# Kernel optimization log

Measured on AMD Instinct MI355X. Metric: run time of the kernel, lower is better.

Reference implementation:

```python
import jax, jax.numpy as jnp
import numpy as np

N_WINDOW = 128  # |i-j| < N_WINDOW kept
D_K = 64

def setup_inputs() -> dict:
    key = jax.random.key(0)
    kq, kk, kv = jax.random.split(key, 3)
    B, H, S, D = 2, 8, 2048, D_K
    Q = jax.random.normal(kq, (B, H, S, D), dtype=jnp.float32)
    K = jax.random.normal(kk, (B, H, S, D), dtype=jnp.float32)
    V = jax.random.normal(kv, (B, H, S, D), dtype=jnp.float32)
    return {"Q": Q, "K": K, "V": V}

def reference(Q, K, V):
    S = Q.shape[-2]
    # scores: [B, H, S, S]
    scores = jnp.einsum('bhqd,bhkd->bhqk', Q, K) / jnp.sqrt(jnp.float32(D_K))
    idx = jnp.arange(S)
    band = jnp.abs(idx[:, None] - idx[None, :]) < N_WINDOW  # [S, S] band mask
    scores = jnp.where(band[None, None, :, :], scores, -jnp.inf)
    attn = jax.nn.softmax(scores, axis=-1)
    context = jnp.einsum('bhqk,bhkd->bhqd', attn, V)
    return (context, attn)
```

## Files before the change

### kernel.cpp

```cpp
#include <hip/hip_runtime.h>
#include <hip/hip_bf16.h>
#include <math.h>

#define S_LEN 2048
#define DK 64
#define TQ 32
#define KLW 320
#define NCH 5
#define PSTR 324
#define PSTR4 81

typedef __attribute__((ext_vector_type(8))) short bf16x8;
typedef __attribute__((ext_vector_type(4))) float f32x4;

__device__ __forceinline__ bf16x8 pack8(f32x4 a, f32x4 b) {
    union { __hip_bfloat162 h[4]; bf16x8 v; } u;
    u.h[0] = __float22bfloat162_rn(make_float2(a[0], a[1]));
    u.h[1] = __float22bfloat162_rn(make_float2(a[2], a[3]));
    u.h[2] = __float22bfloat162_rn(make_float2(b[0], b[1]));
    u.h[3] = __float22bfloat162_rn(make_float2(b[2], b[3]));
    return u.v;
}

__global__ __launch_bounds__(256, 3) void band_attn_v6(
    const float* __restrict__ Q,
    const float* __restrict__ K,
    const float* __restrict__ V,
    float* __restrict__ ctx_out,
    float* __restrict__ attn_out)
{
    __shared__ __align__(16) float Ps[TQ * PSTR];

    const int tid  = threadIdx.x;
    const int bh   = blockIdx.x >> 6;
    const int q0   = (blockIdx.x & 63) * TQ;
    const int base = q0 - 128;

    const int lane = tid & 63;
    const int wv   = tid >> 6;
    const int col  = lane & 15;
    const int quad = lane >> 4;

    const float* Qh = Q + ((size_t)bh * S_LEN + q0) * DK;
    const float* Kh = K + (size_t)bh * S_LEN * DK;
    const float* Vh = V + (size_t)bh * S_LEN * DK;

    bf16x8 qf[2][2];
    #pragma unroll
    for (int qt = 0; qt < 2; ++qt)
        #pragma unroll
        for (int h = 0; h < 2; ++h) {
            const float* qp = Qh + (size_t)(16 * qt + col) * DK + 32 * h + 8 * quad;
            f32x4 a = *(const f32x4*)qp;
            f32x4 b = *(const f32x4*)(qp + 4);
            a *= 0.125f; b *= 0.125f;
            qf[qt][h] = pack8(a, b);
        }

    #pragma unroll
    for (int c = 0; c < NCH; ++c) {
        const int kl  = c * 64 + 16 * wv + col;
        const int kg  = base + kl;
        const int kgc = min(max(kg, 0), S_LEN - 1);
        bf16x8 kf[2];
        #pragma unroll
        for (int h = 0; h < 2; ++h) {
            const float* kp = Kh + (size_t)kgc * DK + 32 * h + 8 * quad;
            kf[h] = pack8(*(const f32x4*)kp, *(const f32x4*)(kp + 4));
        }
        #pragma unroll
        for (int qt = 0; qt < 2; ++qt) {
            f32x4 acc = {0.f, 0.f, 0.f, 0.f};
            acc = __builtin_amdgcn_mfma_f32_16x16x32_bf16(qf[qt][0], kf[0], acc, 0, 0, 0);
            acc = __builtin_amdgcn_mfma_f32_16x16x32_bf16(qf[qt][1], kf[1], acc, 0, 0, 0);
            #pragma unroll
            for (int r = 0; r < 4; ++r) {
                const int qloc = 16 * qt + quad * 4 + r;
                const bool ok = ((unsigned)kg < S_LEN) && (kl > qloc) && (kl <= qloc + 255);
                Ps[qloc * PSTR + kl] = ok ? acc[r] : -INFINITY;
            }
        }
    }

    const int kloff4 = (q0 >> 2) - 32;
    const int L = max(0, kloff4);
    const int R = min(512, kloff4 + (KLW >> 2));
    f32x4* A4w = (f32x4*)(attn_out + ((size_t)bh * S_LEN + q0 + 8 * wv) * S_LEN);
    {
        const f32x4 z = {0.f, 0.f, 0.f, 0.f};
        #pragma unroll
        for (int rr = 0; rr < 8; ++rr) {
            f32x4* row4 = A4w + (size_t)rr * 512;
            for (int s = lane; s < L; s += 64)       row4[s] = z;
            for (int s = R + lane; s < 512; s += 64) row4[s] = z;
        }
    }
    __syncthreads();

    #pragma unroll
    for (int rr = 0; rr < 8; ++rr) {
        float* row = Ps + (wv * 8 + rr) * PSTR;
        float v[5];
        #pragma unroll
        for (int j = 0; j < 5; ++j) v[j] = row[lane + 64 * j];
        float m = fmaxf(fmaxf(fmaxf(v[0], v[1]), fmaxf(v[2], v[3])), v[4]);
        #pragma unroll
        for (int off = 32; off > 0; off >>= 1) m = fmaxf(m, __shfl_xor(m, off, 64));
        float e[5], sum = 0.f;
        #pragma unroll
        for (int j = 0; j < 5; ++j) { e[j] = __expf(v[j] - m); sum += e[j]; }
        #pragma unroll
        for (int off = 32; off > 0; off >>= 1) sum += __shfl_xor(sum, off, 64);
        const float inv = 1.0f / sum;
        #pragma unroll
        for (int j = 0; j < 5; ++j) row[lane + 64 * j] = e[j] * inv;
    }
    __syncthreads();

    f32x4 o0 = {0.f, 0.f, 0.f, 0.f}, o1 = {0.f, 0.f, 0.f, 0.f};
    const float* vcol = Vh + 16 * wv + col;
    #pragma unroll
    for (int c = 0; c < NCH; ++c) {
        #pragma unroll
        for (int h = 0; h < 2; ++h) {
            const int k0 = base + c * 64 + 32 * h + 8 * quad;
            f32x4 va, vb;
            #pragma unroll
            for (int j = 0; j < 4; ++j) {
                int kgc = min(max(k0 + j, 0), S_LEN - 1);
                va[j] = vcol[(size_t)kgc * DK];
            }
            #pragma unroll
            for (int j = 0; j < 4; ++j) {
                int kgc = min(max(k0 + 4 + j, 0), S_LEN - 1);
                vb[j] = vcol[(size_t)kgc * DK];
            }
            bf16x8 vf = pack8(va, vb);
            #pragma unroll
            for (int qt = 0; qt < 2; ++qt) {
                const float* pp = Ps + (size_t)(16 * qt + col) * PSTR + c * 64 + 32 * h + 8 * quad;
                bf16x8 pf = pack8(*(const f32x4*)pp, *(const f32x4*)(pp + 4));
                if (qt == 0) o0 = __builtin_amdgcn_mfma_f32_16x16x32_bf16(pf, vf, o0, 0, 0, 0);
                else         o1 = __builtin_amdgcn_mfma_f32_16x16x32_bf16(pf, vf, o1, 0, 0, 0);
            }
        }
    }

    {
        float* Cg = ctx_out + ((size_t)bh * S_LEN + q0) * DK;
        #pragma unroll
        for (int r = 0; r < 4; ++r) {
            Cg[(size_t)(quad * 4 + r) * DK + 16 * wv + col]      = o0[r];
            Cg[(size_t)(16 + quad * 4 + r) * DK + 16 * wv + col] = o1[r];
        }
    }

    {
        const f32x4* Ps4 = (const f32x4*)Ps;
        #pragma unroll
        for (int rr = 0; rr < 8; ++rr) {
            f32x4* row4 = A4w + (size_t)rr * 512;
            const f32x4* pr = Ps4 + (8 * wv + rr) * PSTR4 - kloff4;
            for (int s = L + lane; s < R; s += 64) row4[s] = pr[s];
        }
    }
}

extern "C" void kernel_launch(void* const* d_in, const int* in_sizes, int n_in,
                              void* d_out, int out_size, void* d_ws, size_t ws_size,
                              hipStream_t stream) {
    const float* Q = (const float*)d_in[0];
    const float* K = (const float*)d_in[1];
    const float* V = (const float*)d_in[2];
    float* out = (float*)d_out;

    const int BH = in_sizes[0] / (S_LEN * DK);
    const size_t ctx_elems = (size_t)BH * S_LEN * DK;
    float* ctx  = out;
    float* attn = out + ctx_elems;

    dim3 grid(BH * (S_LEN / TQ));
    band_attn_v6<<<grid, 256, 0, stream>>>(Q, K, V, ctx, attn);
}
```

Before: 302.8 us.

## Stream band probabilities directly from softmax and stagger zero-fill by block parity

The band probabilities are now written to global memory straight from registers during softmax, using nontemporal scalar stores, instead of a final pass that copied them from shared memory as 16-byte vectors. The zero-fill of the out-of-band attention region also uses nontemporal stores. Odd blocks do this zero-fill before softmax and even blocks after the PV matmul, so write traffic is spread across kernel phases. The cost being targeted is the large attention-matrix write bandwidth and its poor overlap with compute. In exchange, band writes become scalar rather than vector, which may reduce store efficiency.

Measured after the change: 298.3 us. Within noise of the previous version (-1.5%).

```diff
diff --git a/kernel.cpp b/kernel.cpp
--- a/kernel.cpp
+++ b/kernel.cpp
@@ -22,7 +22,7 @@
     return u.v;
 }
 
-__global__ __launch_bounds__(256, 3) void band_attn_v6(
+__global__ __launch_bounds__(256, 3) void band_attn_v7(
     const float* __restrict__ Q,
     const float* __restrict__ K,
     const float* __restrict__ V,
@@ -35,6 +35,7 @@
     const int bh   = blockIdx.x >> 6;
     const int q0   = (blockIdx.x & 63) * TQ;
     const int base = q0 - 128;
+    const int cls  = blockIdx.x & 1;
 
     const int lane = tid & 63;
     const int wv   = tid >> 6;
@@ -44,6 +45,23 @@
     const float* Qh = Q + ((size_t)bh * S_LEN + q0) * DK;
     const float* Kh = K + (size_t)bh * S_LEN * DK;
     const float* Vh = V + (size_t)bh * S_LEN * DK;
+
+    const int kloff4 = (q0 >> 2) - 32;
+    const int L = max(0, kloff4);
+    const int R = min(512, kloff4 + (KLW >> 2));
+    f32x4* A4w = (f32x4*)(attn_out + ((size_t)bh * S_LEN + q0 + 8 * wv) * S_LEN);
+
+    auto store_zeros = [&]() {
+        const f32x4 z = {0.f, 0.f, 0.f, 0.f};
+        #pragma unroll
+        for (int rr = 0; rr < 8; ++rr) {
+            f32x4* row4 = A4w + (size_t)rr * 512;
+            for (int s = lane; s < L; s += 64)
+                __builtin_nontemporal_store(z, row4 + s);
+            for (int s = R + lane; s < 512; s += 64)
+                __builtin_nontemporal_store(z, row4 + s);
+        }
+    };
 
     bf16x8 qf[2][2];
     #pragma unroll
@@ -82,19 +100,7 @@
         }
     }
 
-    const int kloff4 = (q0 >> 2) - 32;
-    const int L = max(0, kloff4);
-    const int R = min(512, kloff4 + (KLW >> 2));
-    f32x4* A4w = (f32x4*)(attn_out + ((size_t)bh * S_LEN + q0 + 8 * wv) * S_LEN);
-    {
-        const f32x4 z = {0.f, 0.f, 0.f, 0.f};
-        #pragma unroll
-        for (int rr = 0; rr < 8; ++rr) {
-            f32x4* row4 = A4w + (size_t)rr * 512;
-            for (int s = lane; s < L; s += 64)       row4[s] = z;
-            for (int s = R + lane; s < 512; s += 64) row4[s] = z;
-        }
-    }
+    if (cls) store_zeros();
     __syncthreads();
 
     #pragma unroll
@@ -112,8 +118,15 @@
         #pragma unroll
         for (int off = 32; off > 0; off >>= 1) sum += __shfl_xor(sum, off, 64);
         const float inv = 1.0f / sum;
+        float* arow = attn_out + ((size_t)bh * S_LEN + q0 + 8 * wv + rr) * S_LEN;
         #pragma unroll
-        for (int j = 0; j < 5; ++j) row[lane + 64 * j] = e[j] * inv;
+        for (int j = 0; j < 5; ++j) {
+            const float p = e[j] * inv;
+            row[lane + 64 * j] = p;
+            const int kg = base + lane + 64 * j;
+            if ((unsigned)kg < S_LEN)
+                __builtin_nontemporal_store(p, arow + kg);
+        }
     }
     __syncthreads();
 
@@ -155,15 +168,7 @@
         }
     }
 
-    {
-        const f32x4* Ps4 = (const f32x4*)Ps;
-        #pragma unroll
-        for (int rr = 0; rr < 8; ++rr) {
-            f32x4* row4 = A4w + (size_t)rr * 512;
-            const f32x4* pr = Ps4 + (8 * wv + rr) * PSTR4 - kloff4;
-            for (int s = L + lane; s < R; s += 64) row4[s] = pr[s];
-        }
-    }
+    if (!cls) store_zeros();
 }
 
 extern "C" void kernel_launch(void* const* d_in, const int* in_sizes, int n_in,
@@ -180,5 +185,5 @@
     float* attn = out + ctx_elems;
 
     dim3 grid(BH * (S_LEN / TQ));
-    band_attn_v6<<<grid, 256, 0, stream>>>(Q, K, V, ctx, attn);
+    band_attn_v7<<<grid, 256, 0, stream>>>(Q, K, V, ctx, attn);
 }
```
